# Optimization experiments

Measured on AMD Instinct MI355X. Metric: run time of the kernel, lower is better.

The kernel has to match this reference:

```python
import jax, jax.numpy as jnp
import numpy as np

B, T, C, H = 32, 1024, 384, 64

def setup_inputs() -> dict:
    key = jax.random.key(0)
    k1, k2, k3, k4 = jax.random.split(key, 4)
    x = jax.random.normal(k1, (B, T, C), dtype=jnp.float32)
    s = 1.0 / np.sqrt(C)
    Wk = jax.random.normal(k2, (C, H), dtype=jnp.float32) * s
    Wq = jax.random.normal(k3, (C, H), dtype=jnp.float32) * s
    Wv = jax.random.normal(k4, (C, H), dtype=jnp.float32) * s
    return {"x": x, "Wk": Wk, "Wq": Wq, "Wv": Wv}

def reference(x, Wk, Wq, Wv):
    # Single-head causal attention (dropout = identity, eval mode).
    Tn = x.shape[1]
    k = jnp.einsum('btc,ch->bth', x, Wk)   # [B,T,H]
    q = jnp.einsum('btc,ch->bth', x, Wq)
    v = jnp.einsum('btc,ch->bth', x, Wv)
    scale = k.shape[-1] ** -0.5
    wei = jnp.einsum('bth,bsh->bts', q, k) * scale  # [B,T,T]
    causal = jnp.tril(jnp.ones((Tn, Tn), dtype=bool))
    wei = jnp.where(causal, wei, -jnp.inf)
    wei = jax.nn.softmax(wei, axis=-1)
    out = jnp.einsum('bts,bsh->bth', wei, v)  # [B,T,H]
    return out
```

## Files before the change

kernel.cpp:

```cpp
#include <hip/hip_runtime.h>

#define BB 32
#define TT 1024
#define CCH 384
#define HH 64

typedef short short8 __attribute__((ext_vector_type(8)));
typedef float f32x4 __attribute__((ext_vector_type(4)));
typedef unsigned short ushort;

static __device__ __forceinline__ ushort f2bf(float f) {
    union { float f; unsigned u; } v; v.f = f;
    unsigned r = v.u + 0x7fff + ((v.u >> 16) & 1);
    return (ushort)(r >> 16);
}

__global__ void wswz(const float* __restrict__ Wk, const float* __restrict__ Wq,
                     const float* __restrict__ Wv, ushort* __restrict__ wf) {
    const int mat = blockIdx.x, ks = blockIdx.y;
    const float* W = (mat == 0) ? Wk : ((mat == 1) ? Wq : Wv);
    const int t = threadIdx.x;
    const int ct = t >> 6, lane = t & 63, quad = lane >> 4, l15 = lane & 15;
    const int col = ct * 16 + l15;
    short8 d;
#pragma unroll
    for (int j = 0; j < 8; ++j)
        d[j] = (short)f2bf(W[(ks * 32 + quad * 8 + j) * 64 + col]);
    *(short8*)(wf + (((mat * 12 + ks) * 4 + ct) << 9) + lane * 8) = d;
}

#define XSTR 388
#define VS_STRIDE 68

__global__ __launch_bounds__(256, 2) void qkv(const float* __restrict__ x,
                                              const ushort* __restrict__ wf,
                                              ushort* __restrict__ kb,
                                              ushort* __restrict__ qb,
                                              ushort* __restrict__ vtb) {
    const int r0 = blockIdx.x * 64;
    const int tid = threadIdx.x;
    const int wv = tid >> 6, lane = tid & 63, l15 = lane & 15, quad = lane >> 4;

    __shared__ ushort xs[64 * XSTR];

#pragma unroll
    for (int kb3 = 0; kb3 < 3; ++kb3) {
        const int kbase = kb3 * 128;
        const int seg = (tid & 7) * 16;
#pragma unroll
        for (int i = 0; i < 2; ++i) {
            const int r = (tid >> 3) + 32 * i;
            const float* src = x + (size_t)(r0 + r) * CCH + kbase + seg;
            f32x4 v0 = *(const f32x4*)(src);
            f32x4 v1 = *(const f32x4*)(src + 4);
            f32x4 v2 = *(const f32x4*)(src + 8);
            f32x4 v3 = *(const f32x4*)(src + 12);
            short8 p0, p1;
#pragma unroll
            for (int j = 0; j < 4; ++j) {
                p0[j]     = (short)f2bf(v0[j]);
                p0[j + 4] = (short)f2bf(v1[j]);
                p1[j]     = (short)f2bf(v2[j]);
                p1[j + 4] = (short)f2bf(v3[j]);
            }
            *(short8*)(xs + r * XSTR + kbase + seg) = p0;
            *(short8*)(xs + r * XSTR + kbase + seg + 8) = p1;
        }
    }
    __syncthreads();

    f32x4 acc[12] = {};
    short8 bf[2][12];
#pragma unroll
    for (int m = 0; m < 3; ++m)
#pragma unroll
        for (int ct = 0; ct < 4; ++ct)
            bf[0][m * 4 + ct] = *(const short8*)(wf + (((m * 12 + 0) * 4 + ct) << 9) + lane * 8);

#pragma unroll
    for (int ks = 0; ks < 12; ++ks) {
        short8 a = *(const short8*)(xs + (wv * 16 + l15) * XSTR + ks * 32 + quad * 8);
        if (ks < 11) {
#pragma unroll
            for (int m = 0; m < 3; ++m)
#pragma unroll
                for (int ct = 0; ct < 4; ++ct)
                    bf[(ks + 1) & 1][m * 4 + ct] =
                        *(const short8*)(wf + (((m * 12 + ks + 1) * 4 + ct) << 9) + lane * 8);
        }
#pragma unroll
        for (int f = 0; f < 12; ++f)
            acc[f] = __builtin_amdgcn_mfma_f32_16x16x32_bf16(a, bf[ks & 1][f], acc[f], 0, 0, 0);
    }

#pragma unroll
    for (int ct = 0; ct < 4; ++ct) {
#pragma unroll
        for (int r = 0; r < 4; ++r) {
            int row = r0 + wv * 16 + quad * 4 + r;
            int col = ct * 16 + l15;
            kb[row * 64 + col] = f2bf(acc[0 + ct][r]);
            qb[row * 64 + col] = f2bf(acc[4 + ct][r]);
        }
    }
    __syncthreads();
    ushort* vs = xs;
#pragma unroll
    for (int ct = 0; ct < 4; ++ct)
#pragma unroll
        for (int r = 0; r < 4; ++r)
            vs[(wv * 16 + quad * 4 + r) * VS_STRIDE + ct * 16 + l15] = f2bf(acc[8 + ct][r]);
    __syncthreads();
    {
        const int col = tid >> 2;
        const int rbase = (tid & 3) * 16;
        short8 d0, d1;
#pragma unroll
        for (int j = 0; j < 8; ++j) {
            d0[j] = (short)vs[(rbase + j) * VS_STRIDE + col];
            d1[j] = (short)vs[(rbase + 8 + j) * VS_STRIDE + col];
        }
        const int b = r0 >> 10;
        const int t = (r0 & 1023) + rbase;
        *(short8*)(vtb + b * 65536 + col * 1024 + t) = d0;
        *(short8*)(vtb + b * 65536 + col * 1024 + t + 8) = d1;
    }
}

#define PSTR 138

__global__ __launch_bounds__(256, 2) void attn(const ushort* __restrict__ qb,
                                               const ushort* __restrict__ kb,
                                               const ushort* __restrict__ vtb,
                                               float* __restrict__ out) {
    const int qt = 15 - blockIdx.y, b = blockIdx.x;
    const int t0 = qt * 64;
    const int tid = threadIdx.x;
    const int wv = tid >> 6, lane = tid & 63, l15 = lane & 15, quad = lane >> 4;

    __shared__ ushort Ks[128 * 72];
    __shared__ ushort Vs[64 * 136];
    __shared__ ushort Ps[4 * 16 * PSTR];
    ushort* Psw = Ps + wv * 16 * PSTR;

    const int qrow = b * 1024 + t0 + wv * 16 + l15;
    short8 qf0 = *(const short8*)(qb + qrow * 64 + quad * 8);
    short8 qf1 = *(const short8*)(qb + qrow * 64 + 32 + quad * 8);

    f32x4 o[4] = {};
    float li[4] = {0.f, 0.f, 0.f, 0.f};
    const float c1 = 0.125f * 1.4426950408889634f;
    const float c2 = 10.0f * 1.4426950408889634f;

    const int nst = (qt >> 1) + 1;

    short8 kr[4], vr[4];
#pragma unroll
    for (int i = 0; i < 4; ++i) {
        int c = tid + i * 256;
        kr[i] = *(const short8*)(kb + (b * 1024 + (c >> 3)) * 64 + (c & 7) * 8);
        vr[i] = *(const short8*)(vtb + b * 65536 + (c >> 4) * 1024 + (c & 15) * 8);
    }

    for (int it = 0; it < nst; ++it) {
        const int s0 = it * 128;
        __syncthreads();
#pragma unroll
        for (int i = 0; i < 4; ++i) {
            int c = tid + i * 256;
            *(short8*)(Ks + (c >> 3) * 72 + (c & 7) * 8) = kr[i];
            *(short8*)(Vs + (c >> 4) * 136 + (c & 15) * 8) = vr[i];
        }
        __syncthreads();
        if (it + 1 < nst) {
            const int sn = s0 + 128;
#pragma unroll
            for (int i = 0; i < 4; ++i) {
                int c = tid + i * 256;
                kr[i] = *(const short8*)(kb + (b * 1024 + sn + (c >> 3)) * 64 + (c & 7) * 8);
                vr[i] = *(const short8*)(vtb + b * 65536 + (c >> 4) * 1024 + sn + (c & 15) * 8);
            }
        }

        f32x4 s[8];
#pragma unroll
        for (int ct = 0; ct < 8; ++ct) {
            f32x4 z = {};
            short8 b0 = *(const short8*)(Ks + (ct * 16 + l15) * 72 + quad * 8);
            z = __builtin_amdgcn_mfma_f32_16x16x32_bf16(qf0, b0, z, 0, 0, 0);
            short8 b1 = *(const short8*)(Ks + (ct * 16 + l15) * 72 + 32 + quad * 8);
            s[ct] = __builtin_amdgcn_mfma_f32_16x16x32_bf16(qf1, b1, z, 0, 0, 0);
        }

        if (it + 1 < nst) {
#pragma unroll
            for (int r = 0; r < 4; ++r) {
#pragma unroll
                for (int ct = 0; ct < 8; ++ct) {
                    float p = exp2f(s[ct][r] * c1 - c2);
                    li[r] += p;
                    Psw[(quad * 4 + r) * PSTR + ct * 16 + l15] = f2bf(p);
                }
            }
        } else {
#pragma unroll
            for (int r = 0; r < 4; ++r) {
                const int trow = t0 + wv * 16 + quad * 4 + r;
#pragma unroll
                for (int ct = 0; ct < 8; ++ct) {
                    int col = s0 + ct * 16 + l15;
                    float p = (col <= trow) ? exp2f(s[ct][r] * c1 - c2) : 0.f;
                    li[r] += p;
                    Psw[(quad * 4 + r) * PSTR + ct * 16 + l15] = f2bf(p);
                }
            }
        }

        short8 pa[4];
#pragma unroll
        for (int kk = 0; kk < 4; ++kk)
            pa[kk] = *(const short8*)(Psw + l15 * PSTR + kk * 32 + quad * 8);

#pragma unroll
        for (int ct = 0; ct < 4; ++ct) {
#pragma unroll
            for (int kk = 0; kk < 4; ++kk) {
                short8 vb = *(const short8*)(Vs + (ct * 16 + l15) * 136 + kk * 32 + quad * 8);
                o[ct] = __builtin_amdgcn_mfma_f32_16x16x32_bf16(pa[kk], vb, o[ct], 0, 0, 0);
            }
        }
    }

#pragma unroll
    for (int r = 0; r < 4; ++r) {
        float rs = li[r];
#pragma unroll
        for (int off = 1; off < 16; off <<= 1)
            rs += __shfl_xor(rs, off);
        float inv = 1.0f / rs;
        int t = t0 + wv * 16 + quad * 4 + r;
#pragma unroll
        for (int ct = 0; ct < 4; ++ct) {
            int h = ct * 16 + l15;
            out[b * 65536 + t * 64 + h] = o[ct][r] * inv;
        }
    }
}

extern "C" void kernel_launch(void* const* d_in, const int* in_sizes, int n_in,
                              void* d_out, int out_size, void* d_ws, size_t ws_size,
                              hipStream_t stream) {
    const float* x  = (const float*)d_in[0];
    const float* Wk = (const float*)d_in[1];
    const float* Wq = (const float*)d_in[2];
    const float* Wv = (const float*)d_in[3];

    char* ws = (char*)d_ws;
    ushort* wf  = (ushort*)ws;
    ushort* kb  = (ushort*)(ws + 256 * 1024);
    ushort* qb  = (ushort*)(ws + 256 * 1024 + 4u * 1024 * 1024);
    ushort* vtb = (ushort*)(ws + 256 * 1024 + 8u * 1024 * 1024);

    wswz<<<dim3(3, 12), dim3(256), 0, stream>>>(Wk, Wq, Wv, wf);
    qkv<<<dim3(512), dim3(256), 0, stream>>>(x, wf, kb, qb, vtb);
    attn<<<dim3(32, 16), dim3(256), 0, stream>>>(qb, kb, vtb, (float*)d_out);
}
```

Measured before the change: 125.4 us.

## Load K and V MFMA fragments directly from global memory, dropping LDS staging

Removes the shared-memory staging buffers for K and V and their register prefetch. Each wave now reads its MFMA B-operand fragments straight from global memory (through L1/L2). This drops two block barriers per iteration and the LDS traffic, and lowers LDS use, which may allow higher occupancy. The cost is that each of the four waves loads the same K/V tiles redundantly, and there is no software prefetch to hide global latency.

```diff
diff --git a/kernel.cpp b/kernel.cpp
--- a/kernel.cpp
+++ b/kernel.cpp
@@ -138,14 +138,15 @@
     const int tid = threadIdx.x;
     const int wv = tid >> 6, lane = tid & 63, l15 = lane & 15, quad = lane >> 4;
 
-    __shared__ ushort Ks[128 * 72];
-    __shared__ ushort Vs[64 * 136];
     __shared__ ushort Ps[4 * 16 * PSTR];
     ushort* Psw = Ps + wv * 16 * PSTR;
 
     const int qrow = b * 1024 + t0 + wv * 16 + l15;
     short8 qf0 = *(const short8*)(qb + qrow * 64 + quad * 8);
     short8 qf1 = *(const short8*)(qb + qrow * 64 + 32 + quad * 8);
+
+    const ushort* kbase = kb + (b * 1024 + l15) * 64 + quad * 8;
+    const ushort* vbase = vtb + b * 65536 + l15 * 1024 + quad * 8;
 
     f32x4 o[4] = {};
     float li[4] = {0.f, 0.f, 0.f, 0.f};
@@ -154,41 +155,17 @@
 
     const int nst = (qt >> 1) + 1;
 
-    short8 kr[4], vr[4];
-#pragma unroll
-    for (int i = 0; i < 4; ++i) {
-        int c = tid + i * 256;
-        kr[i] = *(const short8*)(kb + (b * 1024 + (c >> 3)) * 64 + (c & 7) * 8);
-        vr[i] = *(const short8*)(vtb + b * 65536 + (c >> 4) * 1024 + (c & 15) * 8);
-    }
-
     for (int it = 0; it < nst; ++it) {
         const int s0 = it * 128;
-        __syncthreads();
-#pragma unroll
-        for (int i = 0; i < 4; ++i) {
-            int c = tid + i * 256;
-            *(short8*)(Ks + (c >> 3) * 72 + (c & 7) * 8) = kr[i];
-            *(short8*)(Vs + (c >> 4) * 136 + (c & 15) * 8) = vr[i];
-        }
-        __syncthreads();
-        if (it + 1 < nst) {
-            const int sn = s0 + 128;
-#pragma unroll
-            for (int i = 0; i < 4; ++i) {
-                int c = tid + i * 256;
-                kr[i] = *(const short8*)(kb + (b * 1024 + sn + (c >> 3)) * 64 + (c & 7) * 8);
-                vr[i] = *(const short8*)(vtb + b * 65536 + (c >> 4) * 1024 + sn + (c & 15) * 8);
-            }
-        }
 
         f32x4 s[8];
 #pragma unroll
         for (int ct = 0; ct < 8; ++ct) {
+            const ushort* kf = kbase + (s0 + ct * 16) * 64;
+            short8 b0 = *(const short8*)(kf);
+            short8 b1 = *(const short8*)(kf + 32);
             f32x4 z = {};
-            short8 b0 = *(const short8*)(Ks + (ct * 16 + l15) * 72 + quad * 8);
             z = __builtin_amdgcn_mfma_f32_16x16x32_bf16(qf0, b0, z, 0, 0, 0);
-            short8 b1 = *(const short8*)(Ks + (ct * 16 + l15) * 72 + 32 + quad * 8);
             s[ct] = __builtin_amdgcn_mfma_f32_16x16x32_bf16(qf1, b1, z, 0, 0, 0);
         }
 
@@ -223,10 +200,11 @@
 
 #pragma unroll
         for (int ct = 0; ct < 4; ++ct) {
+            const ushort* vf = vbase + ct * 16384 + s0;
 #pragma unroll
             for (int kk = 0; kk < 4; ++kk) {
-                short8 vb = *(const short8*)(Vs + (ct * 16 + l15) * 136 + kk * 32 + quad * 8);
-                o[ct] = __builtin_amdgcn_mfma_f32_16x16x32_bf16(pa[kk], vb, o[ct], 0, 0, 0);
+                short8 vb8 = *(const short8*)(vf + kk * 32);
+                o[ct] = __builtin_amdgcn_mfma_f32_16x16x32_bf16(pa[kk], vb8, o[ct], 0, 0, 0);
             }
         }
     }
```

Measured after the change: 146.7 us. 1.17x slower.
